# Optimization experiments

Hardware: AMD Instinct MI355X
Metric: run time of the kernel (lower is better)

## Reference

```python
import jax, jax.numpy as jnp
import numpy as np

D_MODEL = 256
D_STATE = 16
D_CONV = 4
EXPAND = 2
D_INNER = EXPAND * D_MODEL  # 512
DT_RANK = (D_MODEL + 15) // 16  # 16


def setup_inputs() -> dict:
    key = jax.random.key(0)
    ks = jax.random.split(key, 8)
    s = 0.02
    x = jax.random.normal(ks[0], (2, D_MODEL, 64, 64), jnp.float32)
    W_in = jax.random.normal(ks[1], (2 * D_INNER, D_MODEL), jnp.float32) * s
    conv_w = jax.random.normal(ks[2], (D_INNER, 1, D_CONV), jnp.float32) * s
    conv_b = jnp.zeros((D_INNER,), jnp.float32)
    W_x = jax.random.normal(ks[3], (DT_RANK + 2 * D_STATE, D_INNER), jnp.float32) * s
    W_dt = jax.random.normal(ks[4], (D_INNER, DT_RANK), jnp.float32) * s
    b_dt = jax.random.normal(ks[5], (D_INNER,), jnp.float32) * 0.1
    A_log = jnp.log(jnp.broadcast_to(jnp.arange(1, D_STATE + 1, dtype=jnp.float32), (D_INNER, D_STATE)))
    Dp = jnp.ones((D_INNER,), jnp.float32)
    W_out = jax.random.normal(ks[6], (D_MODEL, D_INNER), jnp.float32) * s
    return {"x": x, "W_in": W_in, "conv_w": conv_w, "conv_b": conv_b,
            "W_x": W_x, "W_dt": W_dt, "b_dt": b_dt, "A_log": A_log,
            "Dp": Dp, "W_out": W_out}


def _mamba_forward(x, W_in, conv_w, conv_b, W_x, W_dt, b_dt, A_log, Dp, W_out):
    b, c, h, w = x.shape
    L = h * w
    # spatial -> sequence: (B, L, d_model); dropout is identity at inference
    xs = x.reshape(b, c, L).transpose(0, 2, 1)
    # input projection -> (x_in, z), each (B, L, d_inner)
    xz = xs @ W_in.T
    x_in, z = jnp.split(xz, 2, axis=-1)
    # causal depthwise conv over sequence
    xc = x_in.transpose(0, 2, 1)  # (B, D, L)
    xc = jnp.pad(xc, ((0, 0), (0, 0), (D_CONV - 1, 0)))
    xc = jax.lax.conv_general_dilated(
        xc, conv_w, window_strides=(1,), padding='VALID',
        dimension_numbers=('NCH', 'OIH', 'NCH'), feature_group_count=D_INNER)
    xc = xc + conv_b[None, :, None]
    u = jax.nn.silu(xc.transpose(0, 2, 1))  # (B, L, D)
    # input-dependent dt, B, C
    x_dbl = u @ W_x.T  # (B, L, dt_rank + 2*N)
    dt, Bm, Cm = jnp.split(x_dbl, [DT_RANK, DT_RANK + D_STATE], axis=-1)
    dt = jax.nn.softplus(dt @ W_dt.T + b_dt)  # (B, L, D)
    A = -jnp.exp(A_log)  # (D, N)
    dA = jnp.exp(dt[..., None] * A)                         # (B, L, D, N)
    dBu = dt[..., None] * Bm[:, :, None, :] * u[..., None]  # (B, L, D, N)

    def step(h_state, inp):
        dA_t, dBu_t, C_t = inp  # (B,D,N), (B,D,N), (B,N)
        h_state = dA_t * h_state + dBu_t
        y_t = jnp.einsum('bdn,bn->bd', h_state, C_t)
        return h_state, y_t

    h0 = jnp.zeros((b, D_INNER, D_STATE), dtype=x.dtype)
    _, ys = jax.lax.scan(step, h0, (dA.transpose(1, 0, 2, 3),
                                    dBu.transpose(1, 0, 2, 3),
                                    Cm.transpose(1, 0, 2)))
    y = ys.transpose(1, 0, 2)  # (B, L, D)
    y = y + u * Dp
    y = y * jax.nn.silu(z)
    out = y @ W_out.T  # (B, L, d_model)
    return out.transpose(0, 2, 1).reshape(b, c, h, w)


def reference(x, W_in, conv_w, conv_b, W_x, W_dt, b_dt, A_log, Dp, W_out):
    return _mamba_forward(x, W_in, conv_w, conv_b, W_x, W_dt, b_dt, A_log, Dp, W_out)
```

## Files before the change

kernel.cpp:

```cpp
#include <hip/hip_runtime.h>
#include <math.h>

#define L_SEQ 4096
#define BATCH 2
#define BL    8192
#define DM    256
#define DI    512
#define NST   16
#define NCHK  256
#define CLEN  16

typedef float  fx4    __attribute__((ext_vector_type(4)));
typedef __bf16 bf16x8 __attribute__((ext_vector_type(8)));
typedef unsigned short us8 __attribute__((ext_vector_type(8)));

typedef __attribute__((address_space(1))) const void* gptr_t;
typedef __attribute__((address_space(3))) void* lptr_t;

__device__ __forceinline__ void async16(const void* g, void* l) {
    __builtin_amdgcn_global_load_lds((gptr_t)g, (lptr_t)l, 16, 0, 0);
}

__device__ __forceinline__ float fast_sigmoid(float x) {
    return __builtin_amdgcn_rcpf(1.f + __expf(-x));
}

__device__ __forceinline__ unsigned short f2bf(float f) {
    unsigned int u = __float_as_uint(f);
    unsigned int r = u + 0x7fff + ((u >> 16) & 1);
    return (unsigned short)(r >> 16);
}

__device__ __forceinline__ float bf2f(unsigned short s) {
    return __uint_as_float(((unsigned int)s) << 16);
}

__global__ __launch_bounds__(256) void prep(const float* __restrict__ x,
                                            const float* __restrict__ Win,
                                            const float* __restrict__ Wout,
                                            const float* __restrict__ Wx,
                                            unsigned short* __restrict__ xsb,
                                            unsigned short* __restrict__ Winb,
                                            unsigned short* __restrict__ Woutb,
                                            unsigned short* __restrict__ Wxb) {
    const int bx = blockIdx.x;
    const int tid = threadIdx.x;
    if (bx < 512) {
        __shared__ float t[64][65];
        const int b  = bx >> 8;
        const int rem = bx & 255;
        const int c0 = (rem >> 6) * 64;
        const int l0 = (rem & 63) * 64;
        const int lx = tid & 63, cy = tid >> 6;
#pragma unroll
        for (int r = 0; r < 16; ++r) {
            int c = cy * 16 + r;
            t[c][lx] = x[(size_t)(b * DM + c0 + c) * L_SEQ + l0 + lx];
        }
        __syncthreads();
        const int cx = tid & 15, ly = tid >> 4;
#pragma unroll
        for (int r = 0; r < 4; ++r) {
            int l = r * 16 + ly;
            int c = cx * 4;
            ushort4 o;
            o.x = f2bf(t[c + 0][l]);
            o.y = f2bf(t[c + 1][l]);
            o.z = f2bf(t[c + 2][l]);
            o.w = f2bf(t[c + 3][l]);
            *(ushort4*)&xsb[(size_t)(b * L_SEQ + l0 + l) * 256 + c0 + c] = o;
        }
    } else {
        const float4* src;
        ushort4* dst;
        int i;
        if (bx < 768)      { i = (bx - 512) * 256 + tid; src = (const float4*)Win;  dst = (ushort4*)Winb; }
        else if (bx < 896) { i = (bx - 768) * 256 + tid; src = (const float4*)Wout; dst = (ushort4*)Woutb; }
        else               { i = (bx - 896) * 256 + tid; src = (const float4*)Wx;   dst = (ushort4*)Wxb; }
        float4 v = src[i];
        ushort4 o;
        o.x = f2bf(v.x); o.y = f2bf(v.y); o.z = f2bf(v.z); o.w = f2bf(v.w);
        dst[i] = o;
    }
}

__global__ __launch_bounds__(256) void gemm_in_mfma(const unsigned short* __restrict__ Ag,
                                                    const unsigned short* __restrict__ Bg,
                                                    unsigned short* __restrict__ xinb,
                                                    unsigned short* __restrict__ szb) {
    __shared__ __align__(16) unsigned short As[128 * 32];
    __shared__ __align__(16) unsigned short Bs[128 * 32];
    const int tid = threadIdx.x;
    const int lane = tid & 63, w = tid >> 6;
    const int j0 = blockIdx.x * 128;
    const int m0 = blockIdx.y * 128;
    const int srow = lane >> 2;
    const int scol = (lane & 3) * 8;
    const int ln = lane & 15, quad = lane >> 4;
    const int wm = w & 1, wn = w >> 1;

    fx4 acc[4][4];
#pragma unroll
    for (int i = 0; i < 4; ++i)
#pragma unroll
        for (int j = 0; j < 4; ++j) acc[i][j] = (fx4){0.f, 0.f, 0.f, 0.f};

    for (int k0 = 0; k0 < 256; k0 += 32) {
        __syncthreads();
#pragma unroll
        for (int i = 0; i < 2; ++i) {
            int r = w * 32 + i * 16;
            async16(&Ag[(size_t)(m0 + r + srow) * 256 + k0 + scol], &As[(r) * 32]);
            async16(&Bg[(size_t)(j0 + r + srow) * 256 + k0 + scol], &Bs[(r) * 32]);
        }
        __syncthreads();
        bf16x8 af[4], bf[4];
#pragma unroll
        for (int mt = 0; mt < 4; ++mt)
            af[mt] = *(const bf16x8*)&As[(wm * 64 + mt * 16 + ln) * 32 + quad * 8];
#pragma unroll
        for (int nt = 0; nt < 4; ++nt)
            bf[nt] = *(const bf16x8*)&Bs[(wn * 64 + nt * 16 + ln) * 32 + quad * 8];
#pragma unroll
        for (int mt = 0; mt < 4; ++mt)
#pragma unroll
            for (int nt = 0; nt < 4; ++nt)
                acc[mt][nt] = __builtin_amdgcn_mfma_f32_16x16x32_bf16(af[mt], bf[nt], acc[mt][nt], 0, 0, 0);
    }
    const bool is_x = (j0 < 512);
#pragma unroll
    for (int mt = 0; mt < 4; ++mt)
#pragma unroll
        for (int nt = 0; nt < 4; ++nt) {
            int grow = m0 + wm * 64 + mt * 16 + quad * 4;
            int gcol = j0 + wn * 64 + nt * 16 + ln;
#pragma unroll
            for (int r = 0; r < 4; ++r) {
                float v = acc[mt][nt][r];
                if (is_x) {
                    xinb[(size_t)(grow + r) * 512 + gcol] = f2bf(v);
                } else {
                    float s = v * fast_sigmoid(v);
                    szb[(size_t)(grow + r) * 512 + (gcol - 512)] = f2bf(s);
                }
            }
        }
}

__global__ __launch_bounds__(512, 2) void fusedA(const unsigned short* __restrict__ xinb,
                                                 const unsigned short* __restrict__ Wxb,
                                                 const float* __restrict__ cw,
                                                 const float* __restrict__ cb,
                                                 const float* __restrict__ Wdt,
                                                 const float* __restrict__ bdt,
                                                 const float* __restrict__ Alog,
                                                 unsigned short* __restrict__ ub,
                                                 float* __restrict__ xdbl,
                                                 float* __restrict__ dtsum_g,
                                                 float* __restrict__ Cq) {
    __shared__ __align__(16) unsigned short uls[CLEN * 520];
    __shared__ __align__(16) float xdl[CLEN * 48];

    const int tid = threadIdx.x;
    const int bi  = blockIdx.x;
    const int b   = bi >> 8;
    const int ch  = bi & (NCHK - 1);
    const int d   = tid;
    const int lane = tid & 63, w = tid >> 6;
    const int row0 = b * L_SEQ + ch * CLEN;

    const float4 wj = ((const float4*)cw)[d];
    const float bias = cb[d];
    float x0 = 0.f, x1 = 0.f, x2 = 0.f;
    if (ch > 0) {
        x0 = bf2f(xinb[(size_t)(row0 - 3) * 512 + d]);
        x1 = bf2f(xinb[(size_t)(row0 - 2) * 512 + d]);
        x2 = bf2f(xinb[(size_t)(row0 - 1) * 512 + d]);
    }
    float uu[CLEN];
#pragma unroll
    for (int i = 0; i < CLEN; ++i) {
        float xi = bf2f(xinb[(size_t)(row0 + i) * 512 + d]);
        float r = bias;
        r = __fmaf_rn(x0, wj.x, r);
        r = __fmaf_rn(x1, wj.y, r);
        r = __fmaf_rn(x2, wj.z, r);
        r = __fmaf_rn(xi, wj.w, r);
        r = r * fast_sigmoid(r);
        unsigned short rb = f2bf(r);
        uu[i] = bf2f(rb);
        uls[i * 520 + d] = rb;
        ub[(size_t)(row0 + i) * 512 + d] = rb;
        x0 = x1; x1 = x2; x2 = xi;
    }
    __syncthreads();

    if (w < 3) {
        const int ln = lane & 15, quad = lane >> 4;
        const int nt = w;
        fx4 acc = (fx4){0.f, 0.f, 0.f, 0.f};
#pragma unroll
        for (int k0 = 0; k0 < 512; k0 += 32) {
            bf16x8 af = *(const bf16x8*)&uls[ln * 520 + k0 + quad * 8];
            bf16x8 bf = *(const bf16x8*)&Wxb[(size_t)(nt * 16 + ln) * 512 + k0 + quad * 8];
            acc = __builtin_amdgcn_mfma_f32_16x16x32_bf16(af, bf, acc, 0, 0, 0);
        }
#pragma unroll
        for (int r = 0; r < 4; ++r) {
            int m = quad * 4 + r;
            int c = nt * 16 + ln;
            xdl[m * 48 + c] = acc[r];
            xdbl[(size_t)(row0 + m) * 48 + c] = acc[r];
        }
    }
    __syncthreads();

    const fx4 wv0 = *(const fx4*)&Wdt[(size_t)d * NST + 0];
    const fx4 wv1 = *(const fx4*)&Wdt[(size_t)d * NST + 4];
    const fx4 wv2 = *(const fx4*)&Wdt[(size_t)d * NST + 8];
    const fx4 wv3 = *(const fx4*)&Wdt[(size_t)d * NST + 12];
    const float a0 = -__expf(Alog[d * NST]);
    const float bd = bdt[d];

    float h[NST];
#pragma unroll
    for (int n = 0; n < NST; ++n) h[n] = 0.f;
    float dts = 0.f;
#pragma unroll
    for (int i = 0; i < CLEN; ++i) {
        const fx4* xq = (const fx4*)&xdl[i * 48];
        fx4 t0 = xq[0], t1 = xq[1], t2 = xq[2], t3 = xq[3];
        fx4 g0 = xq[4], g1 = xq[5], g2 = xq[6], g3 = xq[7];
        float p0 = __fmaf_rn(t0.y, wv0.y, t0.x * wv0.x);
        p0 = __fmaf_rn(t0.z, wv0.z, p0);
        p0 = __fmaf_rn(t0.w, wv0.w, p0);
        float p1 = __fmaf_rn(t1.y, wv1.y, t1.x * wv1.x);
        p1 = __fmaf_rn(t1.z, wv1.z, p1);
        p1 = __fmaf_rn(t1.w, wv1.w, p1);
        float p2 = __fmaf_rn(t2.y, wv2.y, t2.x * wv2.x);
        p2 = __fmaf_rn(t2.z, wv2.z, p2);
        p2 = __fmaf_rn(t2.w, wv2.w, p2);
        float p3 = __fmaf_rn(t3.y, wv3.y, t3.x * wv3.x);
        p3 = __fmaf_rn(t3.z, wv3.z, p3);
        p3 = __fmaf_rn(t3.w, wv3.w, p3);
        float dtr = bd + ((p0 + p1) + (p2 + p3));
        float dtv = (dtr > 20.f) ? dtr : __logf(1.f + __expf(dtr));
        dts += dtv;
        float bm[NST] = {g0.x, g0.y, g0.z, g0.w, g1.x, g1.y, g1.z, g1.w,
                         g2.x, g2.y, g2.z, g2.w, g3.x, g3.y, g3.z, g3.w};
        float dtu = dtv * uu[i];
        float q  = __expf(dtv * a0);
        float q2 = q * q;
        float dAa = q, dAb = q2;
#pragma unroll
        for (int n = 0; n < NST; n += 2) {
            h[n]     = __fmaf_rn(dAa, h[n],     dtu * bm[n]);
            h[n + 1] = __fmaf_rn(dAb, h[n + 1], dtu * bm[n + 1]);
            dAa *= q2; dAb *= q2;
        }
    }
    dtsum_g[(size_t)(b * NCHK + ch) * 512 + d] = dts;
    const size_t base = (size_t)((b * NCHK + ch) * NST) * 512 + d;
#pragma unroll
    for (int n = 0; n < NST; ++n)
        Cq[base + (size_t)n * 512] = h[n];
}

__global__ __launch_bounds__(512, 1) void scan_phaseB(const float* __restrict__ dtsum_g,
                                                      const float* __restrict__ Cq,
                                                      const float* __restrict__ Alog,
                                                      float* __restrict__ Hin) {
    __shared__ float combS[8 * 64];
    __shared__ float combC[8 * 64];
    const int tid = threadIdx.x;
    const int bi  = blockIdx.x;
    const int b   = bi >> 7;
    const int n   = (bi >> 3) & 15;
    const int dg  = bi & 7;
    const int seg = tid >> 6;
    const int dl  = tid & 63;
    const int d   = dg * 64 + dl;
    const float a = -__expf(Alog[d * NST + n]);

    float ds_r[32], c_r[32];
#pragma unroll
    for (int j = 0; j < 32; ++j) {
        int chb = seg * 32 + j;
        ds_r[j] = dtsum_g[(size_t)(b * NCHK + chb) * 512 + d];
        c_r[j]  = Cq[(size_t)((b * NCHK + chb) * NST + n) * 512 + d];
    }
    float hseg = 0.f, ssum = 0.f;
#pragma unroll
    for (int j = 0; j < 32; ++j) {
        hseg = __fmaf_rn(__expf(ds_r[j] * a), hseg, c_r[j]);
        ssum += ds_r[j];
    }
    combS[seg * 64 + dl] = ssum;
    combC[seg * 64 + dl] = hseg;
    __syncthreads();
    float hpre = 0.f;
    for (int s = 0; s < seg; ++s)
        hpre = __fmaf_rn(__expf(combS[s * 64 + dl] * a), hpre, combC[s * 64 + dl]);
#pragma unroll
    for (int j = 0; j < 32; ++j) {
        int chb = seg * 32 + j;
        Hin[(size_t)((b * NCHK + chb) * NST + n) * 512 + d] = hpre;
        hpre = __fmaf_rn(__expf(ds_r[j] * a), hpre, c_r[j]);
    }
}

__global__ __launch_bounds__(256, 3) void scan_phaseC(const unsigned short* __restrict__ ub,
                                                      const float* __restrict__ xdbl,
                                                      const unsigned short* __restrict__ szb,
                                                      const float* __restrict__ Wdt,
                                                      const float* __restrict__ bdt,
                                                      const float* __restrict__ Alog,
                                                      const float* __restrict__ Dp,
                                                      const float* __restrict__ Hin,
                                                      unsigned short* __restrict__ ygb) {
    const int tid = threadIdx.x;
    const int bidx = blockIdx.x;
    const int dhalf = bidx & 1;
    const int ch = (bidx >> 1) & (NCHK - 1);
    const int b = bidx >> 9;
    const int d = dhalf * 256 + tid;

    const fx4 wv0 = *(const fx4*)&Wdt[(size_t)d * NST + 0];
    const fx4 wv1 = *(const fx4*)&Wdt[(size_t)d * NST + 4];
    const fx4 wv2 = *(const fx4*)&Wdt[(size_t)d * NST + 8];
    const fx4 wv3 = *(const fx4*)&Wdt[(size_t)d * NST + 12];
    const float a0 = -__expf(Alog[d * NST]);
    const float bd = bdt[d];
    const float dp = Dp[d];
    const int row0 = b * L_SEQ + ch * CLEN;

    float uu[CLEN], sz[CLEN];
#pragma unroll
    for (int i = 0; i < CLEN; ++i)
        uu[i] = bf2f(ub[(size_t)(row0 + i) * 512 + d]);
#pragma unroll
    for (int i = 0; i < CLEN; ++i)
        sz[i] = bf2f(szb[(size_t)(row0 + i) * 512 + d]);

    const size_t hbase = (size_t)((b * NCHK + ch) * NST) * 512 + d;
    float h[NST];
#pragma unroll
    for (int n = 0; n < NST; ++n) h[n] = Hin[hbase + (size_t)n * 512];

#pragma unroll
    for (int i = 0; i < CLEN; ++i) {
        const fx4* xq = (const fx4*)&xdbl[(size_t)(row0 + i) * 48];
        fx4 t0 = xq[0], t1 = xq[1], t2 = xq[2], t3 = xq[3];
        fx4 g0 = xq[4], g1 = xq[5], g2 = xq[6], g3 = xq[7];
        fx4 c0 = xq[8], c1 = xq[9], c2 = xq[10], c3 = xq[11];
        float p0 = __fmaf_rn(t0.y, wv0.y, t0.x * wv0.x);
        p0 = __fmaf_rn(t0.z, wv0.z, p0);
        p0 = __fmaf_rn(t0.w, wv0.w, p0);
        float p1 = __fmaf_rn(t1.y, wv1.y, t1.x * wv1.x);
        p1 = __fmaf_rn(t1.z, wv1.z, p1);
        p1 = __fmaf_rn(t1.w, wv1.w, p1);
        float p2 = __fmaf_rn(t2.y, wv2.y, t2.x * wv2.x);
        p2 = __fmaf_rn(t2.z, wv2.z, p2);
        p2 = __fmaf_rn(t2.w, wv2.w, p2);
        float p3 = __fmaf_rn(t3.y, wv3.y, t3.x * wv3.x);
        p3 = __fmaf_rn(t3.z, wv3.z, p3);
        p3 = __fmaf_rn(t3.w, wv3.w, p3);
        float dtr = bd + ((p0 + p1) + (p2 + p3));
        float dtv = (dtr > 20.f) ? dtr : __logf(1.f + __expf(dtr));
        float bm[NST] = {g0.x, g0.y, g0.z, g0.w, g1.x, g1.y, g1.z, g1.w,
                         g2.x, g2.y, g2.z, g2.w, g3.x, g3.y, g3.z, g3.w};
        float cm[NST] = {c0.x, c0.y, c0.z, c0.w, c1.x, c1.y, c1.z, c1.w,
                         c2.x, c2.y, c2.z, c2.w, c3.x, c3.y, c3.z, c3.w};
        float dtu = dtv * uu[i];
        float q  = __expf(dtv * a0);
        float q2 = q * q;
        float dAa = q, dAb = q2;
        float y0 = 0.f, y1 = 0.f;
#pragma unroll
        for (int n = 0; n < NST; n += 2) {
            h[n]     = __fmaf_rn(dAa, h[n],     dtu * bm[n]);
            h[n + 1] = __fmaf_rn(dAb, h[n + 1], dtu * bm[n + 1]);
            y0 = __fmaf_rn(h[n],     cm[n],     y0);
            y1 = __fmaf_rn(h[n + 1], cm[n + 1], y1);
            dAa *= q2; dAb *= q2;
        }
        float y = y0 + y1;
        ygb[(size_t)(row0 + i) * 512 + d] = f2bf((y + uu[i] * dp) * sz[i]);
    }
}

__global__ __launch_bounds__(256) void gemm_out_mfma(const unsigned short* __restrict__ Ag,
                                                     const unsigned short* __restrict__ Bg,
                                                     float* __restrict__ out) {
    __shared__ __align__(16) unsigned short As[64 * 32];
    __shared__ __align__(16) unsigned short Bs[128 * 32];
    const int tid = threadIdx.x;
    const int lane = tid & 63, w = tid >> 6;
    const int m0 = blockIdx.x * 64;
    const int l0 = blockIdx.y * 128;
    const int srow = lane >> 2;
    const int scol = (lane & 3) * 8;
    const int ln = lane & 15, quad = lane >> 4;

    fx4 acc[4][2];
#pragma unroll
    for (int i = 0; i < 4; ++i) {
        acc[i][0] = (fx4){0.f, 0.f, 0.f, 0.f};
        acc[i][1] = (fx4){0.f, 0.f, 0.f, 0.f};
    }

    for (int k0 = 0; k0 < 512; k0 += 32) {
        __syncthreads();
        {
            int ra = w * 16;
            async16(&Ag[(size_t)(m0 + ra + srow) * 512 + k0 + scol], &As[ra * 32]);
#pragma unroll
            for (int i = 0; i < 2; ++i) {
                int rb = w * 32 + i * 16;
                async16(&Bg[(size_t)(l0 + rb + srow) * 512 + k0 + scol], &Bs[rb * 32]);
            }
        }
        __syncthreads();
        bf16x8 af[4], bf[2];
#pragma unroll
        for (int mt = 0; mt < 4; ++mt)
            af[mt] = *(const bf16x8*)&As[(mt * 16 + ln) * 32 + quad * 8];
#pragma unroll
        for (int nt = 0; nt < 2; ++nt)
            bf[nt] = *(const bf16x8*)&Bs[(w * 32 + nt * 16 + ln) * 32 + quad * 8];
#pragma unroll
        for (int mt = 0; mt < 4; ++mt)
#pragma unroll
            for (int nt = 0; nt < 2; ++nt)
                acc[mt][nt] = __builtin_amdgcn_mfma_f32_16x16x32_bf16(af[mt], bf[nt], acc[mt][nt], 0, 0, 0);
    }
#pragma unroll
    for (int mt = 0; mt < 4; ++mt)
#pragma unroll
        for (int nt = 0; nt < 2; ++nt) {
            int mrow = m0 + mt * 16 + quad * 4;
            int bl = l0 + w * 32 + nt * 16 + ln;
            int b = bl >> 12, l = bl & 4095;
#pragma unroll
            for (int r = 0; r < 4; ++r)
                out[(size_t)(b * DM + mrow + r) * L_SEQ + l] = acc[mt][nt][r];
        }
}

extern "C" void kernel_launch(void* const* d_in, const int* in_sizes, int n_in,
                              void* d_out, int out_size, void* d_ws, size_t ws_size,
                              hipStream_t stream) {
    const float* x    = (const float*)d_in[0];
    const float* Win  = (const float*)d_in[1];
    const float* cw   = (const float*)d_in[2];
    const float* cb   = (const float*)d_in[3];
    const float* Wx   = (const float*)d_in[4];
    const float* Wdt  = (const float*)d_in[5];
    const float* bdt  = (const float*)d_in[6];
    const float* Alog = (const float*)d_in[7];
    const float* Dp   = (const float*)d_in[8];
    const float* Wout = (const float*)d_in[9];
    float* out = (float*)d_out;

    float* ws     = (float*)d_ws;
    float* xinb_f = ws;
    float* ub_f   = xinb_f + 2097152;
    float* szb_f  = ub_f   + 2097152;
    float* ygb_f  = szb_f  + 2097152;
    float* xdbl   = ygb_f  + 2097152;
    float* dtsum  = xdbl   + 393216;
    float* Cq     = dtsum  + 262144;
    float* Hin    = Cq     + 4194304;
    float* xsb_f  = Hin    + 4194304;
    float* Winb_f = xsb_f  + 1048576;
    float* Wob_f  = Winb_f + 131072;
    float* Wxb_f  = Wob_f  + 65536;

    unsigned short* xinb  = (unsigned short*)xinb_f;
    unsigned short* ub    = (unsigned short*)ub_f;
    unsigned short* szb   = (unsigned short*)szb_f;
    unsigned short* ygb   = (unsigned short*)ygb_f;
    unsigned short* xsb   = (unsigned short*)xsb_f;
    unsigned short* Winb  = (unsigned short*)Winb_f;
    unsigned short* Woutb = (unsigned short*)Wob_f;
    unsigned short* Wxb   = (unsigned short*)Wxb_f;

    prep<<<dim3(920), 256, 0, stream>>>(x, Win, Wout, Wx, xsb, Winb, Woutb, Wxb);
    gemm_in_mfma<<<dim3(8, 64), 256, 0, stream>>>(xsb, Winb, xinb, szb);
    fusedA<<<dim3(BATCH * NCHK), 512, 0, stream>>>(xinb, Wxb, cw, cb, Wdt, bdt, Alog,
                                                   ub, xdbl, dtsum, Cq);
    scan_phaseB<<<dim3(256), 512, 0, stream>>>(dtsum, Cq, Alog, Hin);
    scan_phaseC<<<dim3(BATCH * NCHK * 2), 256, 0, stream>>>(ub, xdbl, szb, Wdt, bdt, Alog, Dp, Hin, ygb);
    gemm_out_mfma<<<dim3(4, 64), 256, 0, stream>>>(Woutb, ygb, out);
}
```

Measured before the change: 147.3 us.

## Fuse fp32-to-bf16 conversion into GEMM loads and drop prep kernel

Removes the separate prep kernel that transposed x and converted weights to bf16. The input GEMM now reads fp32 x and W_in directly, converting and transposing in registers before writing to LDS. fusedA and gemm_out instead convert W_x and W_out on the fly from global fp32. scan_phaseB is also reshaped to 1024 threads with 16 chunks per segment, which halves the serial work per thread at the cost of a longer cross-segment combine. This saves a launch and an intermediate round trip, but gives up the async global-to-LDS loads for synchronous register-staged loads.

```diff
diff --git a/kernel.cpp b/kernel.cpp
--- a/kernel.cpp
+++ b/kernel.cpp
@@ -12,6 +12,7 @@
 
 typedef float  fx4    __attribute__((ext_vector_type(4)));
 typedef __bf16 bf16x8 __attribute__((ext_vector_type(8)));
+typedef __bf16 bf16x4 __attribute__((ext_vector_type(4)));
 typedef unsigned short us8 __attribute__((ext_vector_type(8)));
 
 typedef __attribute__((address_space(1))) const void* gptr_t;
@@ -35,57 +36,15 @@
     return __uint_as_float(((unsigned int)s) << 16);
 }
 
-__global__ __launch_bounds__(256) void prep(const float* __restrict__ x,
-                                            const float* __restrict__ Win,
-                                            const float* __restrict__ Wout,
-                                            const float* __restrict__ Wx,
-                                            unsigned short* __restrict__ xsb,
-                                            unsigned short* __restrict__ Winb,
-                                            unsigned short* __restrict__ Woutb,
-                                            unsigned short* __restrict__ Wxb) {
-    const int bx = blockIdx.x;
-    const int tid = threadIdx.x;
-    if (bx < 512) {
-        __shared__ float t[64][65];
-        const int b  = bx >> 8;
-        const int rem = bx & 255;
-        const int c0 = (rem >> 6) * 64;
-        const int l0 = (rem & 63) * 64;
-        const int lx = tid & 63, cy = tid >> 6;
-#pragma unroll
-        for (int r = 0; r < 16; ++r) {
-            int c = cy * 16 + r;
-            t[c][lx] = x[(size_t)(b * DM + c0 + c) * L_SEQ + l0 + lx];
-        }
-        __syncthreads();
-        const int cx = tid & 15, ly = tid >> 4;
-#pragma unroll
-        for (int r = 0; r < 4; ++r) {
-            int l = r * 16 + ly;
-            int c = cx * 4;
-            ushort4 o;
-            o.x = f2bf(t[c + 0][l]);
-            o.y = f2bf(t[c + 1][l]);
-            o.z = f2bf(t[c + 2][l]);
-            o.w = f2bf(t[c + 3][l]);
-            *(ushort4*)&xsb[(size_t)(b * L_SEQ + l0 + l) * 256 + c0 + c] = o;
-        }
-    } else {
-        const float4* src;
-        ushort4* dst;
-        int i;
-        if (bx < 768)      { i = (bx - 512) * 256 + tid; src = (const float4*)Win;  dst = (ushort4*)Winb; }
-        else if (bx < 896) { i = (bx - 768) * 256 + tid; src = (const float4*)Wout; dst = (ushort4*)Woutb; }
-        else               { i = (bx - 896) * 256 + tid; src = (const float4*)Wx;   dst = (ushort4*)Wxb; }
-        float4 v = src[i];
-        ushort4 o;
-        o.x = f2bf(v.x); o.y = f2bf(v.y); o.z = f2bf(v.z); o.w = f2bf(v.w);
-        dst[i] = o;
-    }
-}
-
-__global__ __launch_bounds__(256) void gemm_in_mfma(const unsigned short* __restrict__ Ag,
-                                                    const unsigned short* __restrict__ Bg,
+__device__ __forceinline__ bf16x8 cvt8(float4 a, float4 b) {
+    bf16x8 r;
+    r[0] = (__bf16)a.x; r[1] = (__bf16)a.y; r[2] = (__bf16)a.z; r[3] = (__bf16)a.w;
+    r[4] = (__bf16)b.x; r[5] = (__bf16)b.y; r[6] = (__bf16)b.z; r[7] = (__bf16)b.w;
+    return r;
+}
+
+__global__ __launch_bounds__(256) void gemm_in_mfma(const float* __restrict__ x,
+                                                    const float* __restrict__ Win,
                                                     unsigned short* __restrict__ xinb,
                                                     unsigned short* __restrict__ szb) {
     __shared__ __align__(16) unsigned short As[128 * 32];
@@ -94,10 +53,14 @@
     const int lane = tid & 63, w = tid >> 6;
     const int j0 = blockIdx.x * 128;
     const int m0 = blockIdx.y * 128;
-    const int srow = lane >> 2;
-    const int scol = (lane & 3) * 8;
+    const int xb  = m0 >> 12;
+    const int xl0 = m0 & 4095;
     const int ln = lane & 15, quad = lane >> 4;
     const int wm = w & 1, wn = w >> 1;
+    const int ac0 = (tid & 7) * 4;
+    const int ar0 = (tid >> 3) * 4;
+    const int bjr = tid >> 1;
+    const int bkh = (tid & 1) * 16;
 
     fx4 acc[4][4];
 #pragma unroll
@@ -107,11 +70,22 @@
 
     for (int k0 = 0; k0 < 256; k0 += 32) {
         __syncthreads();
-#pragma unroll
-        for (int i = 0; i < 2; ++i) {
-            int r = w * 32 + i * 16;
-            async16(&Ag[(size_t)(m0 + r + srow) * 256 + k0 + scol], &As[(r) * 32]);
-            async16(&Bg[(size_t)(j0 + r + srow) * 256 + k0 + scol], &Bs[(r) * 32]);
+        float La[4][4], Lb[4][4];
+#pragma unroll
+        for (int j = 0; j < 4; ++j)
+            *(float4*)La[j] = *(const float4*)&x[((size_t)(xb * DM + k0 + ac0 + j)) * L_SEQ + xl0 + ar0];
+#pragma unroll
+        for (int j = 0; j < 4; ++j)
+            *(float4*)Lb[j] = *(const float4*)&Win[(size_t)(j0 + bjr) * 256 + k0 + bkh + 4 * j];
+#pragma unroll
+        for (int r = 0; r < 4; ++r) {
+            bf16x4 o = { (__bf16)La[0][r], (__bf16)La[1][r], (__bf16)La[2][r], (__bf16)La[3][r] };
+            *(bf16x4*)&As[(ar0 + r) * 32 + ac0] = o;
+        }
+#pragma unroll
+        for (int j = 0; j < 4; ++j) {
+            bf16x4 o = { (__bf16)Lb[j][0], (__bf16)Lb[j][1], (__bf16)Lb[j][2], (__bf16)Lb[j][3] };
+            *(bf16x4*)&Bs[bjr * 32 + bkh + 4 * j] = o;
         }
         __syncthreads();
         bf16x8 af[4], bf[4];
@@ -148,7 +122,7 @@
 }
 
 __global__ __launch_bounds__(512, 2) void fusedA(const unsigned short* __restrict__ xinb,
-                                                 const unsigned short* __restrict__ Wxb,
+                                                 const float* __restrict__ Wx,
                                                  const float* __restrict__ cw,
                                                  const float* __restrict__ cb,
                                                  const float* __restrict__ Wdt,
@@ -198,12 +172,14 @@
     if (w < 3) {
         const int ln = lane & 15, quad = lane >> 4;
         const int nt = w;
+        const float* wrow = &Wx[(size_t)(nt * 16 + ln) * 512];
         fx4 acc = (fx4){0.f, 0.f, 0.f, 0.f};
 #pragma unroll
         for (int k0 = 0; k0 < 512; k0 += 32) {
             bf16x8 af = *(const bf16x8*)&uls[ln * 520 + k0 + quad * 8];
-            bf16x8 bf = *(const bf16x8*)&Wxb[(size_t)(nt * 16 + ln) * 512 + k0 + quad * 8];
-            acc = __builtin_amdgcn_mfma_f32_16x16x32_bf16(af, bf, acc, 0, 0, 0);
+            float4 wa = *(const float4*)&wrow[k0 + quad * 8];
+            float4 wb = *(const float4*)&wrow[k0 + quad * 8 + 4];
+            acc = __builtin_amdgcn_mfma_f32_16x16x32_bf16(af, cvt8(wa, wb), acc, 0, 0, 0);
         }
 #pragma unroll
         for (int r = 0; r < 4; ++r) {
@@ -266,12 +242,12 @@
         Cq[base + (size_t)n * 512] = h[n];
 }
 
-__global__ __launch_bounds__(512, 1) void scan_phaseB(const float* __restrict__ dtsum_g,
-                                                      const float* __restrict__ Cq,
-                                                      const float* __restrict__ Alog,
-                                                      float* __restrict__ Hin) {
-    __shared__ float combS[8 * 64];
-    __shared__ float combC[8 * 64];
+__global__ __launch_bounds__(1024, 1) void scan_phaseB(const float* __restrict__ dtsum_g,
+                                                       const float* __restrict__ Cq,
+                                                       const float* __restrict__ Alog,
+                                                       float* __restrict__ Hin) {
+    __shared__ float combS[16 * 64];
+    __shared__ float combC[16 * 64];
     const int tid = threadIdx.x;
     const int bi  = blockIdx.x;
     const int b   = bi >> 7;
@@ -282,16 +258,16 @@
     const int d   = dg * 64 + dl;
     const float a = -__expf(Alog[d * NST + n]);
 
-    float ds_r[32], c_r[32];
-#pragma unroll
-    for (int j = 0; j < 32; ++j) {
-        int chb = seg * 32 + j;
+    float ds_r[16], c_r[16];
+#pragma unroll
+    for (int j = 0; j < 16; ++j) {
+        int chb = seg * 16 + j;
         ds_r[j] = dtsum_g[(size_t)(b * NCHK + chb) * 512 + d];
         c_r[j]  = Cq[(size_t)((b * NCHK + chb) * NST + n) * 512 + d];
     }
     float hseg = 0.f, ssum = 0.f;
 #pragma unroll
-    for (int j = 0; j < 32; ++j) {
+    for (int j = 0; j < 16; ++j) {
         hseg = __fmaf_rn(__expf(ds_r[j] * a), hseg, c_r[j]);
         ssum += ds_r[j];
     }
@@ -302,8 +278,8 @@
     for (int s = 0; s < seg; ++s)
         hpre = __fmaf_rn(__expf(combS[s * 64 + dl] * a), hpre, combC[s * 64 + dl]);
 #pragma unroll
-    for (int j = 0; j < 32; ++j) {
-        int chb = seg * 32 + j;
+    for (int j = 0; j < 16; ++j) {
+        int chb = seg * 16 + j;
         Hin[(size_t)((b * NCHK + chb) * NST + n) * 512 + d] = hpre;
         hpre = __fmaf_rn(__expf(ds_r[j] * a), hpre, c_r[j]);
     }
@@ -389,10 +365,9 @@
     }
 }
 
-__global__ __launch_bounds__(256) void gemm_out_mfma(const unsigned short* __restrict__ Ag,
+__global__ __launch_bounds__(256) void gemm_out_mfma(const float* __restrict__ Wout,
                                                      const unsigned short* __restrict__ Bg,
                                                      float* __restrict__ out) {
-    __shared__ __align__(16) unsigned short As[64 * 32];
     __shared__ __align__(16) unsigned short Bs[128 * 32];
     const int tid = threadIdx.x;
     const int lane = tid & 63, w = tid >> 6;
@@ -411,20 +386,19 @@
 
     for (int k0 = 0; k0 < 512; k0 += 32) {
         __syncthreads();
-        {
-            int ra = w * 16;
-            async16(&Ag[(size_t)(m0 + ra + srow) * 512 + k0 + scol], &As[ra * 32]);
-#pragma unroll
-            for (int i = 0; i < 2; ++i) {
-                int rb = w * 32 + i * 16;
-                async16(&Bg[(size_t)(l0 + rb + srow) * 512 + k0 + scol], &Bs[rb * 32]);
-            }
+#pragma unroll
+        for (int i = 0; i < 2; ++i) {
+            int rb = w * 32 + i * 16;
+            async16(&Bg[(size_t)(l0 + rb + srow) * 512 + k0 + scol], &Bs[rb * 32]);
+        }
+        bf16x8 af[4];
+#pragma unroll
+        for (int mt = 0; mt < 4; ++mt) {
+            const float* wr = &Wout[(size_t)(m0 + mt * 16 + ln) * 512 + k0 + quad * 8];
+            af[mt] = cvt8(*(const float4*)wr, *(const float4*)(wr + 4));
         }
         __syncthreads();
-        bf16x8 af[4], bf[2];
-#pragma unroll
-        for (int mt = 0; mt < 4; ++mt)
-            af[mt] = *(const bf16x8*)&As[(mt * 16 + ln) * 32 + quad * 8];
+        bf16x8 bf[2];
 #pragma unroll
         for (int nt = 0; nt < 2; ++nt)
             bf[nt] = *(const bf16x8*)&Bs[(w * 32 + nt * 16 + ln) * 32 + quad * 8];
@@ -471,25 +445,16 @@
     float* dtsum  = xdbl   + 393216;
     float* Cq     = dtsum  + 262144;
     float* Hin    = Cq     + 4194304;
-    float* xsb_f  = Hin    + 4194304;
-    float* Winb_f = xsb_f  + 1048576;
-    float* Wob_f  = Winb_f + 131072;
-    float* Wxb_f  = Wob_f  + 65536;
 
     unsigned short* xinb  = (unsigned short*)xinb_f;
     unsigned short* ub    = (unsigned short*)ub_f;
     unsigned short* szb   = (unsigned short*)szb_f;
     unsigned short* ygb   = (unsigned short*)ygb_f;
-    unsigned short* xsb   = (unsigned short*)xsb_f;
-    unsigned short* Winb  = (unsigned short*)Winb_f;
-    unsigned short* Woutb = (unsigned short*)Wob_f;
-    unsigned short* Wxb   = (unsigned short*)Wxb_f;
-
-    prep<<<dim3(920), 256, 0, stream>>>(x, Win, Wout, Wx, xsb, Winb, Woutb, Wxb);
-    gemm_in_mfma<<<dim3(8, 64), 256, 0, stream>>>(xsb, Winb, xinb, szb);
-    fusedA<<<dim3(BATCH * NCHK), 512, 0, stream>>>(xinb, Wxb, cw, cb, Wdt, bdt, Alog,
+
+    gemm_in_mfma<<<dim3(8, 64), 256, 0, stream>>>(x, Win, xinb, szb);
+    fusedA<<<dim3(BATCH * NCHK), 512, 0, stream>>>(xinb, Wx, cw, cb, Wdt, bdt, Alog,
                                                    ub, xdbl, dtsum, Cq);
-    scan_phaseB<<<dim3(256), 512, 0, stream>>>(dtsum, Cq, Alog, Hin);
+    scan_phaseB<<<dim3(256), 1024, 0, stream>>>(dtsum, Cq, Alog, Hin);
     scan_phaseC<<<dim3(BATCH * NCHK * 2), 256, 0, stream>>>(ub, xdbl, szb, Wdt, bdt, Alog, Dp, Hin, ygb);
-    gemm_out_mfma<<<dim3(4, 64), 256, 0, stream>>>(Woutb, ygb, out);
-}
+    gemm_out_mfma<<<dim3(4, 64), 256, 0, stream>>>(Wout, ygb, out);
+}
```

Result: slower. 174.4 us (+18.4%).

## Recompute conv+SiLU in scan phase C and widen phase B to 16 segments

Applied to the files above, without the earlier changes.

fusedA no longer writes the bf16 u tensor to global memory. scan_phaseC now rebuilds u from xinb by redoing the causal depthwise conv and SiLU, which removes an 8 MB write and read of u at the cost of a few extra loads and FMAs per element. Separately, scan_phaseB now runs 1024 threads per block with 16 segments of 16 chunks each, which halves the serial chunk loop per thread and doubles the parallelism of the inter-chunk scan. The inter-segment prefix loop becomes longer in exchange.

```diff
diff --git a/kernel.cpp b/kernel.cpp
--- a/kernel.cpp
+++ b/kernel.cpp
@@ -12,6 +12,7 @@
 
 typedef float  fx4    __attribute__((ext_vector_type(4)));
 typedef __bf16 bf16x8 __attribute__((ext_vector_type(8)));
+typedef __bf16 bf16x4 __attribute__((ext_vector_type(4)));
 typedef unsigned short us8 __attribute__((ext_vector_type(8)));
 
 typedef __attribute__((address_space(1))) const void* gptr_t;
@@ -154,7 +155,6 @@
                                                  const float* __restrict__ Wdt,
                                                  const float* __restrict__ bdt,
                                                  const float* __restrict__ Alog,
-                                                 unsigned short* __restrict__ ub,
                                                  float* __restrict__ xdbl,
                                                  float* __restrict__ dtsum_g,
                                                  float* __restrict__ Cq) {
@@ -190,7 +190,6 @@
         unsigned short rb = f2bf(r);
         uu[i] = bf2f(rb);
         uls[i * 520 + d] = rb;
-        ub[(size_t)(row0 + i) * 512 + d] = rb;
         x0 = x1; x1 = x2; x2 = xi;
     }
     __syncthreads();
@@ -266,12 +265,12 @@
         Cq[base + (size_t)n * 512] = h[n];
 }
 
-__global__ __launch_bounds__(512, 1) void scan_phaseB(const float* __restrict__ dtsum_g,
-                                                      const float* __restrict__ Cq,
-                                                      const float* __restrict__ Alog,
-                                                      float* __restrict__ Hin) {
-    __shared__ float combS[8 * 64];
-    __shared__ float combC[8 * 64];
+__global__ __launch_bounds__(1024, 1) void scan_phaseB(const float* __restrict__ dtsum_g,
+                                                       const float* __restrict__ Cq,
+                                                       const float* __restrict__ Alog,
+                                                       float* __restrict__ Hin) {
+    __shared__ float combS[16 * 64];
+    __shared__ float combC[16 * 64];
     const int tid = threadIdx.x;
     const int bi  = blockIdx.x;
     const int b   = bi >> 7;
@@ -282,16 +281,16 @@
     const int d   = dg * 64 + dl;
     const float a = -__expf(Alog[d * NST + n]);
 
-    float ds_r[32], c_r[32];
-#pragma unroll
-    for (int j = 0; j < 32; ++j) {
-        int chb = seg * 32 + j;
+    float ds_r[16], c_r[16];
+#pragma unroll
+    for (int j = 0; j < 16; ++j) {
+        int chb = seg * 16 + j;
         ds_r[j] = dtsum_g[(size_t)(b * NCHK + chb) * 512 + d];
         c_r[j]  = Cq[(size_t)((b * NCHK + chb) * NST + n) * 512 + d];
     }
     float hseg = 0.f, ssum = 0.f;
 #pragma unroll
-    for (int j = 0; j < 32; ++j) {
+    for (int j = 0; j < 16; ++j) {
         hseg = __fmaf_rn(__expf(ds_r[j] * a), hseg, c_r[j]);
         ssum += ds_r[j];
     }
@@ -302,16 +301,18 @@
     for (int s = 0; s < seg; ++s)
         hpre = __fmaf_rn(__expf(combS[s * 64 + dl] * a), hpre, combC[s * 64 + dl]);
 #pragma unroll
-    for (int j = 0; j < 32; ++j) {
-        int chb = seg * 32 + j;
+    for (int j = 0; j < 16; ++j) {
+        int chb = seg * 16 + j;
         Hin[(size_t)((b * NCHK + chb) * NST + n) * 512 + d] = hpre;
         hpre = __fmaf_rn(__expf(ds_r[j] * a), hpre, c_r[j]);
     }
 }
 
-__global__ __launch_bounds__(256, 3) void scan_phaseC(const unsigned short* __restrict__ ub,
+__global__ __launch_bounds__(256, 3) void scan_phaseC(const unsigned short* __restrict__ xinb,
                                                       const float* __restrict__ xdbl,
                                                       const unsigned short* __restrict__ szb,
+                                                      const float* __restrict__ cw,
+                                                      const float* __restrict__ cb,
                                                       const float* __restrict__ Wdt,
                                                       const float* __restrict__ bdt,
                                                       const float* __restrict__ Alog,
@@ -334,10 +335,27 @@
     const float dp = Dp[d];
     const int row0 = b * L_SEQ + ch * CLEN;
 
+    const float4 wj = ((const float4*)cw)[d];
+    const float bias = cb[d];
+    float x0 = 0.f, x1 = 0.f, x2 = 0.f;
+    if (ch > 0) {
+        x0 = bf2f(xinb[(size_t)(row0 - 3) * 512 + d]);
+        x1 = bf2f(xinb[(size_t)(row0 - 2) * 512 + d]);
+        x2 = bf2f(xinb[(size_t)(row0 - 1) * 512 + d]);
+    }
     float uu[CLEN], sz[CLEN];
 #pragma unroll
-    for (int i = 0; i < CLEN; ++i)
-        uu[i] = bf2f(ub[(size_t)(row0 + i) * 512 + d]);
+    for (int i = 0; i < CLEN; ++i) {
+        float xi = bf2f(xinb[(size_t)(row0 + i) * 512 + d]);
+        float r = bias;
+        r = __fmaf_rn(x0, wj.x, r);
+        r = __fmaf_rn(x1, wj.y, r);
+        r = __fmaf_rn(x2, wj.z, r);
+        r = __fmaf_rn(xi, wj.w, r);
+        r = r * fast_sigmoid(r);
+        uu[i] = bf2f(f2bf(r));
+        x0 = x1; x1 = x2; x2 = xi;
+    }
 #pragma unroll
     for (int i = 0; i < CLEN; ++i)
         sz[i] = bf2f(szb[(size_t)(row0 + i) * 512 + d]);
@@ -464,8 +482,7 @@
 
     float* ws     = (float*)d_ws;
     float* xinb_f = ws;
-    float* ub_f   = xinb_f + 2097152;
-    float* szb_f  = ub_f   + 2097152;
+    float* szb_f  = xinb_f + 2097152;
     float* ygb_f  = szb_f  + 2097152;
     float* xdbl   = ygb_f  + 2097152;
     float* dtsum  = xdbl   + 393216;
@@ -477,7 +494,6 @@
     float* Wxb_f  = Wob_f  + 65536;
 
     unsigned short* xinb  = (unsigned short*)xinb_f;
-    unsigned short* ub    = (unsigned short*)ub_f;
     unsigned short* szb   = (unsigned short*)szb_f;
     unsigned short* ygb   = (unsigned short*)ygb_f;
     unsigned short* xsb   = (unsigned short*)xsb_f;
@@ -488,8 +504,9 @@
     prep<<<dim3(920), 256, 0, stream>>>(x, Win, Wout, Wx, xsb, Winb, Woutb, Wxb);
     gemm_in_mfma<<<dim3(8, 64), 256, 0, stream>>>(xsb, Winb, xinb, szb);
     fusedA<<<dim3(BATCH * NCHK), 512, 0, stream>>>(xinb, Wxb, cw, cb, Wdt, bdt, Alog,
-                                                   ub, xdbl, dtsum, Cq);
-    scan_phaseB<<<dim3(256), 512, 0, stream>>>(dtsum, Cq, Alog, Hin);
-    scan_phaseC<<<dim3(BATCH * NCHK * 2), 256, 0, stream>>>(ub, xdbl, szb, Wdt, bdt, Alog, Dp, Hin, ygb);
+                                                   xdbl, dtsum, Cq);
+    scan_phaseB<<<dim3(256), 1024, 0, stream>>>(dtsum, Cq, Alog, Hin);
+    scan_phaseC<<<dim3(BATCH * NCHK * 2), 256, 0, stream>>>(xinb, xdbl, szb, cw, cb,
+                                                            Wdt, bdt, Alog, Dp, Hin, ygb);
     gemm_out_mfma<<<dim3(4, 64), 256, 0, stream>>>(Woutb, ygb, out);
 }
```

Result: no change. 149.5 us (+1.5%).
